# Optimization experiments

Measured on AMD Instinct MI355X. Metric: run time of the kernel, lower is better.

## Reference

```python
import jax, jax.numpy as jnp
import numpy as np

N_HEAD = 16
OUTPUT_DIM = 1024
HEAD_DIM = OUTPUT_DIM // N_HEAD  # 64


def setup_inputs() -> dict:
    key = jax.random.key(0)
    kq, kk, kv = jax.random.split(key, 3)
    B, S, D = 4, 2048, OUTPUT_DIM
    return {
        "Q": jax.random.normal(kq, (B, S, D), dtype=jnp.float32),
        "K": jax.random.normal(kk, (B, S, D), dtype=jnp.float32),
        "V": jax.random.normal(kv, (B, S, D), dtype=jnp.float32),
    }


def reference(Q, K, V):
    # FAITHFUL to the original Keras layer: it reshapes Q into K and V as well
    # (K = reshape(Q, ...), V = reshape(Q, ...)), so the K and V inputs are
    # ignored and attention is computed of Q against itself.
    B, S, _ = Q.shape
    q = Q.reshape(B, S, N_HEAD, HEAD_DIM)  # [B,S,H,D]
    scale = 1.0 / np.sqrt(HEAD_DIM).astype(np.float32)
    # scores: [B,H,S,S]
    scores = jnp.einsum("bshd,bthd->bhst", q, q) * scale
    attn = jax.nn.softmax(scores, axis=-1)
    out = jnp.einsum("bhst,bthd->bshd", attn, q)  # [B,S,H,D]
    # concat of per-head slices along last axis == head-major reshape
    return out.reshape(B, S, N_HEAD * HEAD_DIM)
```

## Files before the change

kernel.cpp:

```cpp
#include <hip/hip_runtime.h>
#include <stdint.h>

#define S_LEN 2048
#define DH    64
#define NH    16
#define DM    1024
#define NBH   64
#define PP    72

typedef float    f32x4 __attribute__((ext_vector_type(4)));
typedef _Float16 half8 __attribute__((ext_vector_type(8)));
typedef _Float16 half4 __attribute__((ext_vector_type(4)));

__global__ __launch_bounds__(256) void preprocess_kernel(const float* __restrict__ Q,
                                                         _Float16* __restrict__ Qh,
                                                         _Float16* __restrict__ QhT) {
    __shared__ _Float16 T[DH * 68];
    const int tid = threadIdx.x;
    const int st = blockIdx.x & 31;
    const int bh = blockIdx.x >> 5;
    const int b = bh >> 4, h = bh & 15;
    const float* src = Q + (size_t)b * S_LEN * DM + (size_t)(st * 64) * DM + h * DH;
    _Float16* qh_dst = Qh + ((size_t)bh * S_LEN + st * 64) * DH;
    _Float16* qt_dst = QhT + (size_t)bh * DH * S_LEN + st * 64;

    #pragma unroll
    for (int i = 0; i < 4; ++i) {
        const int lin = i * 256 + tid;
        const int sr  = lin >> 4;
        const int d4  = (lin & 15) * 4;
        const float4 v = *(const float4*)(src + (size_t)sr * DM + d4);
        const half4 hv = { (_Float16)v.x, (_Float16)v.y, (_Float16)v.z, (_Float16)v.w };
        *(half4*)(qh_dst + sr * DH + d4) = hv;
        T[(d4 + 0) * 68 + sr] = hv[0];
        T[(d4 + 1) * 68 + sr] = hv[1];
        T[(d4 + 2) * 68 + sr] = hv[2];
        T[(d4 + 3) * 68 + sr] = hv[3];
    }
    __syncthreads();
    #pragma unroll
    for (int i = 0; i < 4; ++i) {
        const int lin = i * 256 + tid;
        const int d   = lin >> 4;
        const int s4  = (lin & 15) * 4;
        const half4 tv = *(const half4*)&T[d * 68 + s4];
        *(half4*)(qt_dst + (size_t)d * S_LEN + s4) = tv;
    }
}

__global__ __launch_bounds__(128, 2) void attn_v7_kernel(const _Float16* __restrict__ Qh,
                                                         const _Float16* __restrict__ QhT,
                                                         float* __restrict__ out) {
    __shared__ __align__(16) _Float16 Pbuf[2 * 64 * PP];

    const int tid  = threadIdx.x;
    const int w    = tid >> 6;
    const int lane = tid & 63;
    const int quad = lane >> 4;
    const int l15  = lane & 15;

    const int bi   = blockIdx.x;
    const int xcd  = bi & 7;
    const int slot = bi >> 3;
    const int bh   = xcd * 8 + (slot >> 4);
    const int qblk = slot & 15;
    const int q0   = qblk * 128 + w * 64;

    const _Float16* qh_bh = Qh + (size_t)bh * S_LEN * DH;
    const _Float16* qt_bh = QhT + (size_t)bh * DH * S_LEN;

    half8 qreg[4][2];
    #pragma unroll
    for (int nch = 0; nch < 4; ++nch) {
        const _Float16* p = qh_bh + (size_t)(q0 + nch * 16 + l15) * DH + quad * 8;
        qreg[nch][0] = *(const half8*)p;
        qreg[nch][1] = *(const half8*)(p + 32);
    }

    const float qs = 0.18033688011112042f;
    float m_c[4];
    #pragma unroll
    for (int nch = 0; nch < 4; ++nch) {
        float part = 0.f;
        #pragma unroll
        for (int s = 0; s < 2; ++s)
            #pragma unroll
            for (int j = 0; j < 8; ++j) { const float x = (float)qreg[nch][s][j]; part += x * x; }
        part += __shfl_xor(part, 16, 64);
        part += __shfl_xor(part, 32, 64);
        m_c[nch] = qs * part;
    }

    half8 ones;
    #pragma unroll
    for (int j = 0; j < 8; ++j) ones[j] = (_Float16)1.0f;

    f32x4 O[4][4];
    #pragma unroll
    for (int a = 0; a < 4; ++a)
        #pragma unroll
        for (int n = 0; n < 4; ++n) O[a][n] = (f32x4){0.f, 0.f, 0.f, 0.f};
    f32x4 Lacc[4];
    #pragma unroll
    for (int a = 0; a < 4; ++a) Lacc[a] = (f32x4){0.f, 0.f, 0.f, 0.f};

    _Float16* Pw = &Pbuf[w * 64 * PP];
    const _Float16* knA = qh_bh + (size_t)(l15)*DH + quad * 8;
    const _Float16* vtA = qt_bh + (size_t)(l15)*S_LEN + quad * 8;

    for (int t = 0; t < 32; ++t) {
        #pragma unroll
        for (int mch = 0; mch < 4; ++mch) {
            const _Float16* kp = knA + (size_t)(t * 64 + mch * 16) * DH;
            const half8 a0 = *(const half8*)kp;
            const half8 a1 = *(const half8*)(kp + 32);
            #pragma unroll
            for (int nch = 0; nch < 4; ++nch) {
                f32x4 acc = (f32x4){0.f, 0.f, 0.f, 0.f};
                acc = __builtin_amdgcn_mfma_f32_16x16x32_f16(a0, qreg[nch][0], acc, 0, 0, 0);
                acc = __builtin_amdgcn_mfma_f32_16x16x32_f16(a1, qreg[nch][1], acc, 0, 0, 0);
                const float p0 = __builtin_amdgcn_exp2f(__builtin_fmaf(acc[0], qs, -m_c[nch]));
                const float p1 = __builtin_amdgcn_exp2f(__builtin_fmaf(acc[1], qs, -m_c[nch]));
                const float p2 = __builtin_amdgcn_exp2f(__builtin_fmaf(acc[2], qs, -m_c[nch]));
                const float p3 = __builtin_amdgcn_exp2f(__builtin_fmaf(acc[3], qs, -m_c[nch]));
                const half4 hv = (half4){ (_Float16)p0, (_Float16)p1, (_Float16)p2, (_Float16)p3 };
                *(half4*)&Pw[(nch * 16 + l15) * PP + mch * 16 + quad * 4] = hv;
            }
        }

        half8 pf[4][2];
        #pragma unroll
        for (int a = 0; a < 4; ++a) {
            pf[a][0] = *(const half8*)&Pw[(a * 16 + l15) * PP + quad * 8];
            pf[a][1] = *(const half8*)&Pw[(a * 16 + l15) * PP + 32 + quad * 8];
        }

        #pragma unroll
        for (int a = 0; a < 4; ++a) {
            Lacc[a] = __builtin_amdgcn_mfma_f32_16x16x32_f16(pf[a][0], ones, Lacc[a], 0, 0, 0);
            Lacc[a] = __builtin_amdgcn_mfma_f32_16x16x32_f16(pf[a][1], ones, Lacc[a], 0, 0, 0);
        }

        #pragma unroll
        for (int nch = 0; nch < 4; ++nch) {
            const _Float16* vp = vtA + (size_t)(nch * 16) * S_LEN + t * 64;
            const half8 v0 = *(const half8*)vp;
            const half8 v1 = *(const half8*)(vp + 32);
            #pragma unroll
            for (int a = 0; a < 4; ++a) {
                O[a][nch] = __builtin_amdgcn_mfma_f32_16x16x32_f16(pf[a][0], v0, O[a][nch], 0, 0, 0);
                O[a][nch] = __builtin_amdgcn_mfma_f32_16x16x32_f16(pf[a][1], v1, O[a][nch], 0, 0, 0);
            }
        }
    }

    const int b = bh >> 4, h = bh & 15;
    float* ob = out + (size_t)b * S_LEN * DM + h * DH;
    #pragma unroll
    for (int a = 0; a < 4; ++a) {
        float inv[4];
        #pragma unroll
        for (int r = 0; r < 4; ++r) inv[r] = 1.0f / Lacc[a][r];
        #pragma unroll
        for (int nch = 0; nch < 4; ++nch)
            #pragma unroll
            for (int r = 0; r < 4; ++r)
                ob[(size_t)(q0 + a * 16 + quad * 4 + r) * DM + nch * 16 + l15] = O[a][nch][r] * inv[r];
    }
}

extern "C" void kernel_launch(void* const* d_in, const int* in_sizes, int n_in,
                              void* d_out, int out_size, void* d_ws, size_t ws_size,
                              hipStream_t stream) {
    const float* Q = (const float*)d_in[0];
    float* out = (float*)d_out;
    _Float16* Qh  = (_Float16*)d_ws;
    _Float16* QhT = Qh + (size_t)NBH * S_LEN * DH;
    preprocess_kernel<<<dim3(NBH * (S_LEN / 64)), dim3(256), 0, stream>>>(Q, Qh, QhT);
    attn_v7_kernel<<<dim3(NBH * (S_LEN / 128)), dim3(128), 0, stream>>>(Qh, QhT, out);
}
```

Baseline: 245.4 us.

## Split key range across the two waves and reduce partial outputs in LDS

Each block now handles 64 queries, with its two waves processing disjoint halves of the key sequence instead of separate query tiles. Wave 1 writes its partial output (as fp16) and row sums into shared memory, and wave 0 adds them before normalizing and storing. This doubles the grid size to improve occupancy and load balance, at the cost of an extra LDS reduction, a barrier, and fp16 rounding of partial accumulators.

```diff
diff --git a/kernel.cpp b/kernel.cpp
--- a/kernel.cpp
+++ b/kernel.cpp
@@ -48,7 +48,7 @@
     }
 }
 
-__global__ __launch_bounds__(128, 2) void attn_v7_kernel(const _Float16* __restrict__ Qh,
+__global__ __launch_bounds__(128, 2) void attn_v8_kernel(const _Float16* __restrict__ Qh,
                                                          const _Float16* __restrict__ QhT,
                                                          float* __restrict__ out) {
     __shared__ __align__(16) _Float16 Pbuf[2 * 64 * PP];
@@ -62,9 +62,10 @@
     const int bi   = blockIdx.x;
     const int xcd  = bi & 7;
     const int slot = bi >> 3;
-    const int bh   = xcd * 8 + (slot >> 4);
-    const int qblk = slot & 15;
-    const int q0   = qblk * 128 + w * 64;
+    const int bh   = xcd * 8 + (slot >> 5);
+    const int qblk = slot & 31;
+    const int q0   = qblk * 64;
+    const int kb   = w * (S_LEN / 2);
 
     const _Float16* qh_bh = Qh + (size_t)bh * S_LEN * DH;
     const _Float16* qt_bh = QhT + (size_t)bh * DH * S_LEN;
@@ -105,10 +106,10 @@
     for (int a = 0; a < 4; ++a) Lacc[a] = (f32x4){0.f, 0.f, 0.f, 0.f};
 
     _Float16* Pw = &Pbuf[w * 64 * PP];
-    const _Float16* knA = qh_bh + (size_t)(l15)*DH + quad * 8;
-    const _Float16* vtA = qt_bh + (size_t)(l15)*S_LEN + quad * 8;
-
-    for (int t = 0; t < 32; ++t) {
+    const _Float16* knA = qh_bh + (size_t)(kb + l15) * DH + quad * 8;
+    const _Float16* vtA = qt_bh + (size_t)l15 * S_LEN + kb + quad * 8;
+
+    for (int t = 0; t < 16; ++t) {
         #pragma unroll
         for (int mch = 0; mch < 4; ++mch) {
             const _Float16* kp = knA + (size_t)(t * 64 + mch * 16) * DH;
@@ -154,18 +155,46 @@
         }
     }
 
-    const int b = bh >> 4, h = bh & 15;
-    float* ob = out + (size_t)b * S_LEN * DM + h * DH;
-    #pragma unroll
-    for (int a = 0; a < 4; ++a) {
-        float inv[4];
-        #pragma unroll
-        for (int r = 0; r < 4; ++r) inv[r] = 1.0f / Lacc[a][r];
-        #pragma unroll
-        for (int nch = 0; nch < 4; ++nch)
+    _Float16* obx = &Pbuf[64 * PP];
+    float*    Lx  = (float*)&Pbuf[64 * PP + 64 * 68];
+    if (w == 1) {
+        #pragma unroll
+        for (int a = 0; a < 4; ++a) {
+            #pragma unroll
+            for (int nch = 0; nch < 4; ++nch)
+                #pragma unroll
+                for (int r = 0; r < 4; ++r)
+                    obx[(a * 16 + quad * 4 + r) * 68 + nch * 16 + l15] = (_Float16)O[a][nch][r];
+            if (l15 == 0)
+                #pragma unroll
+                for (int r = 0; r < 4; ++r)
+                    Lx[a * 16 + quad * 4 + r] = Lacc[a][r];
+        }
+    }
+    __syncthreads();
+    if (w == 0) {
+        #pragma unroll
+        for (int a = 0; a < 4; ++a)
+            #pragma unroll
+            for (int nch = 0; nch < 4; ++nch)
+                #pragma unroll
+                for (int r = 0; r < 4; ++r)
+                    O[a][nch][r] += (float)obx[(a * 16 + quad * 4 + r) * 68 + nch * 16 + l15];
+
+        const int b = bh >> 4, h = bh & 15;
+        float* ob = out + (size_t)b * S_LEN * DM + h * DH;
+        #pragma unroll
+        for (int a = 0; a < 4; ++a) {
+            float inv[4];
             #pragma unroll
             for (int r = 0; r < 4; ++r)
-                ob[(size_t)(q0 + a * 16 + quad * 4 + r) * DM + nch * 16 + l15] = O[a][nch][r] * inv[r];
+                inv[r] = 1.0f / (Lacc[a][r] + Lx[a * 16 + quad * 4 + r]);
+            #pragma unroll
+            for (int nch = 0; nch < 4; ++nch)
+                #pragma unroll
+                for (int r = 0; r < 4; ++r)
+                    ob[(size_t)(q0 + a * 16 + quad * 4 + r) * DM + nch * 16 + l15] = O[a][nch][r] * inv[r];
+        }
     }
 }
 
@@ -177,5 +206,5 @@
     _Float16* Qh  = (_Float16*)d_ws;
     _Float16* QhT = Qh + (size_t)NBH * S_LEN * DH;
     preprocess_kernel<<<dim3(NBH * (S_LEN / 64)), dim3(256), 0, stream>>>(Q, Qh, QhT);
-    attn_v7_kernel<<<dim3(NBH * (S_LEN / 128)), dim3(128), 0, stream>>>(Qh, QhT, out);
+    attn_v8_kernel<<<dim3(NBH * (S_LEN / 64)), dim3(128), 0, stream>>>(Qh, QhT, out);
 }
```

New measurement: 252.1 us. 1.03x slower.
